# Kernel optimization log

Measured on AMD Instinct MI355X. Metric: run time of the kernel, lower is better.

Reference implementation:

```python
import jax, jax.numpy as jnp
import numpy as np

B, T, D, H, C = 32, 160, 512, 256, 6625  # batch, time, feat, gru hidden, num classes


def _gru_scan(x_proj, rk, rbias):
    """Keras GRU (reset_after=True) over time.
    x_proj: [T, B, 3H] = x @ kernel + input_bias (precomputed).
    rk: [H, 3H] recurrent kernel, rbias: [3H] recurrent bias.
    Returns hidden states [T, B, H]."""
    h0 = jnp.zeros((x_proj.shape[1], rk.shape[0]), dtype=x_proj.dtype)

    def step(h, xp):
        inner = h @ rk + rbias                 # [B, 3H]
        xz, xr, xh = jnp.split(xp, 3, axis=-1)
        rz, rr, rh = jnp.split(inner, 3, axis=-1)
        z = jax.nn.sigmoid(xz + rz)            # update gate
        r = jax.nn.sigmoid(xr + rr)            # reset gate
        hh = jnp.tanh(xh + r * rh)             # candidate
        hn = z * h + (1.0 - z) * hh
        return hn, hn

    _, hs = jax.lax.scan(step, h0, x_proj)
    return hs  # [T, B, H]


def setup_inputs() -> dict:
    key = jax.random.key(0)
    ks = jax.random.split(key, 9)
    s_in, s_rec, s_cls = 1.0 / np.sqrt(D), 1.0 / np.sqrt(H), 0.1
    return {
        "x": jax.random.normal(ks[0], (B, T, D), jnp.float32),
        "kernel_fwd": jax.random.normal(ks[1], (D, 3 * H), jnp.float32) * s_in,
        "rk_fwd": jax.random.normal(ks[2], (H, 3 * H), jnp.float32) * s_rec,
        "bias_fwd": jnp.zeros((2, 3 * H), jnp.float32),
        "kernel_bwd": jax.random.normal(ks[3], (D, 3 * H), jnp.float32) * s_in,
        "rk_bwd": jax.random.normal(ks[4], (H, 3 * H), jnp.float32) * s_rec,
        "bias_bwd": jnp.zeros((2, 3 * H), jnp.float32),
        "W": jax.random.truncated_normal(ks[5], -2.0, 2.0, (2 * H, C), jnp.float32) * s_cls,
        "b": jnp.zeros((C,), jnp.float32),
    }


def reference(x, kernel_fwd, rk_fwd, bias_fwd, kernel_bwd, rk_bwd, bias_bwd, W, b):
    x_t = jnp.transpose(x, (1, 0, 2))                       # [T, B, D]
    # forward direction
    xp_f = x_t @ kernel_fwd + bias_fwd[0]                   # [T, B, 3H]
    h_f = _gru_scan(xp_f, rk_fwd, bias_fwd[1])              # [T, B, H]
    # backward direction: run on time-reversed input, reverse output
    x_rev = x_t[::-1]
    xp_b = x_rev @ kernel_bwd + bias_bwd[0]
    h_b = _gru_scan(xp_b, rk_bwd, bias_bwd[1])[::-1]        # [T, B, H]
    out = jnp.concatenate([h_f, h_b], axis=-1)              # [T, B, 2H]
    # classifier applied per position; original reshape/matmul/reshape/transpose
    # ([B,T,2H]->[-1,2H]@W -> [B,T,C] -> [T,B,C]) is equivalent to this:
    logits = out @ W + b                                    # [T, B, C]
    return logits
```

## Files before the change

kernel.cpp:

```cpp
#include <hip/hip_runtime.h>
#include <hip/hip_bf16.h>


#define B 32
#define T 160
#define D 512
#define H 256
#define C 6625
#define H3 768
#define NT16 416
#define KP_PER_DIR 393216
#define RKB_PER_DIR 196608

typedef __attribute__((ext_vector_type(8))) short short8v;
typedef __attribute__((ext_vector_type(4))) float float4v;

__device__ inline unsigned short f2bf(float v) {
    __hip_bfloat16 b = __float2bfloat16(v);
    return *reinterpret_cast<unsigned short*>(&b);
}

__global__ __launch_bounds__(256) void pack_rkB_kernel(
    const float* __restrict__ rkf, const float* __restrict__ rkb,
    unsigned short* __restrict__ rkB)
{
    const int idx = blockIdx.x * 256 + threadIdx.x;
    const int dir = blockIdx.y;
    const float* rk = dir ? rkb : rkf;
    const int i   = idx & 7;
    const int col = (idx >> 3) & 15;
    const int kc  = (idx >> 7) & 31;
    const int nt  = idx >> 12;
    rkB[dir * RKB_PER_DIR + idx] = f2bf(rk[(kc * 8 + i) * H3 + nt * 16 + col]);
}

__global__ __launch_bounds__(256) void pack_W_kernel(
    const float* __restrict__ W, unsigned short* __restrict__ Wp)
{
    const int idx = blockIdx.x * 256 + threadIdx.x;
    const int i   = idx & 7;
    const int col = (idx >> 3) & 15;
    const int kc  = (idx >> 7) & 63;
    const int nt  = idx >> 13;
    const int k = kc * 8 + i;
    const int c = nt * 16 + col;
    const float v = (c < C) ? W[k * C + c] : 0.f;
    Wp[idx] = f2bf(v);
}

__global__ __launch_bounds__(256) void pack_xb_kernel(
    const float* __restrict__ x, unsigned short* __restrict__ xb)
{
    const int idx = blockIdx.x * 256 + threadIdx.x;
    const int k   = idx & 511;
    const int row = idx >> 9;
    const int t   = row >> 5;
    const int b   = row & 31;
    xb[idx] = f2bf(x[(b * T + t) * 512 + k]);
}

__global__ __launch_bounds__(256) void pack_kern_kernel(
    const float* __restrict__ kf, const float* __restrict__ kb,
    unsigned short* __restrict__ kernP)
{
    const int idx = blockIdx.x * 256 + threadIdx.x;
    const int dir = blockIdx.y;
    const float* kern = dir ? kb : kf;
    const int i   = idx & 7;
    const int col = (idx >> 3) & 15;
    const int kc  = (idx >> 7) & 63;
    const int nt  = idx >> 13;
    kernP[dir * KP_PER_DIR + idx] = f2bf(kern[(kc * 8 + i) * H3 + nt * 16 + col]);
}

__global__ __launch_bounds__(256) void proj_mfma_kernel(
    const unsigned short* __restrict__ xb,
    const unsigned short* __restrict__ kernP,
    const float* __restrict__ bias_f,
    const float* __restrict__ bias_b,
    float* __restrict__ xp)
{
    const int bid = blockIdx.x;
    const int ct  = bid / 40;
    const int rt  = bid % 40;
    const int dir = blockIdx.y;
    const int lane = threadIdx.x & 63;
    const int wid  = threadIdx.x >> 6;
    const int wm = wid >> 1, wn = wid & 1;
    const int rowBase = rt * 128 + wm * 64;
    const int lrow = lane & 15;
    const int lk8  = lane >> 4;
    const float* bias = dir ? bias_b : bias_f;

    float4v acc[4][4];
#pragma unroll
    for (int i = 0; i < 4; ++i)
#pragma unroll
        for (int k = 0; k < 4; ++k) acc[i][k] = (float4v){0.f, 0.f, 0.f, 0.f};

    const short* A  = (const short*)xb;
    const short* Bp = (const short*)(kernP + dir * KP_PER_DIR);
    const int ntBase = ct * 8 + wn * 4;

    int arow[4];
#pragma unroll
    for (int mt = 0; mt < 4; ++mt) {
        const int r0 = rowBase + mt * 16;
        const int s  = r0 >> 5;
        arow[mt] = (dir ? (159 - s) : s) * 32 + (r0 & 31);
    }

    for (int k0 = 0; k0 < 512; k0 += 32) {
        short8v aF[4], bF[4];
#pragma unroll
        for (int mt = 0; mt < 4; ++mt)
            aF[mt] = *(const short8v*)&A[(arow[mt] + lrow) * 512 + k0 + lk8 * 8];
#pragma unroll
        for (int ntw = 0; ntw < 4; ++ntw)
            bF[ntw] = *(const short8v*)&Bp[((ntBase + ntw) * 64 + (k0 >> 3) + lk8) * 128 + lrow * 8];
#pragma unroll
        for (int mt = 0; mt < 4; ++mt)
#pragma unroll
            for (int ntw = 0; ntw < 4; ++ntw)
                acc[mt][ntw] = __builtin_amdgcn_mfma_f32_16x16x32_bf16(
                    aF[mt], bF[ntw], acc[mt][ntw], 0, 0, 0);
    }

    const int orow = (lane >> 4) * 4;
#pragma unroll
    for (int ntw = 0; ntw < 4; ++ntw) {
        const int c = (ntBase + ntw) * 16 + lrow;
        const float bc = bias[c];
#pragma unroll
        for (int mt = 0; mt < 4; ++mt)
#pragma unroll
            for (int v = 0; v < 4; ++v)
                xp[(size_t)(dir * 5120 + rowBase + mt * 16 + orow + v) * H3 + c]
                    = acc[mt][ntw][v] + bc;
    }
}

__global__ __launch_bounds__(768, 3) void gru_scan_v6(
    const float* __restrict__ xp,
    const unsigned short* __restrict__ rkB,
    const float* __restrict__ bias_f,
    const float* __restrict__ bias_b,
    __hip_bfloat16* __restrict__ hcatb)
{
    const int bid = blockIdx.x;
    const int dir = bid >> 5;
    const int b   = bid & 31;
    const int tid = threadIdx.x;
    const int wv  = tid >> 6;
    const int lane = tid & 63;
    const int lrow = lane & 15;
    const int lk8  = lane >> 4;
    const int j   = tid & 255;
    const float* bias = dir ? bias_b : bias_f;
    const short* Bp = (const short*)(rkB + (size_t)dir * RKB_PER_DIR);

    short8v bw[32];
#pragma unroll
    for (int i = 0; i < 4; ++i)
#pragma unroll
        for (int kk = 0; kk < 8; ++kk)
            bw[i * 8 + kk] = *(const short8v*)
                &Bp[(((wv * 4 + i) * 32) + kk * 4 + lk8) * 128 + lrow * 8];

    float rbz = 0.f, rbr = 0.f, rbh = 0.f;
    if (tid < 256) {
        rbz = bias[H3 + j];
        rbr = bias[H3 + 256 + j];
        rbh = bias[H3 + 512 + j];
    }

    __shared__ float hfp[256];
    __shared__ __align__(16) unsigned short hus[256];
    __shared__ float sums[768];
    if (tid < 256) { hfp[tid] = 0.f; hus[tid] = 0; }
    __syncthreads();

    for (int s = 0; s < T; ++s) {
        float xz = 0.f, xr = 0.f, xh = 0.f;
        if (tid < 256) {
            const float* xrow = xp + ((dir * T + s) * B + b) * H3;
            xz = xrow[j];
            xr = xrow[256 + j];
            xh = xrow[512 + j];
        }

        float4v a0 = {0.f,0.f,0.f,0.f}, a1 = {0.f,0.f,0.f,0.f};
        float4v a2 = {0.f,0.f,0.f,0.f}, a3 = {0.f,0.f,0.f,0.f};
#pragma unroll
        for (int kk = 0; kk < 8; ++kk) {
            short8v aF = *(const short8v*)&hus[kk * 32 + lk8 * 8];
            a0 = __builtin_amdgcn_mfma_f32_16x16x32_bf16(aF, bw[0 * 8 + kk], a0, 0, 0, 0);
            a1 = __builtin_amdgcn_mfma_f32_16x16x32_bf16(aF, bw[1 * 8 + kk], a1, 0, 0, 0);
            a2 = __builtin_amdgcn_mfma_f32_16x16x32_bf16(aF, bw[2 * 8 + kk], a2, 0, 0, 0);
            a3 = __builtin_amdgcn_mfma_f32_16x16x32_bf16(aF, bw[3 * 8 + kk], a3, 0, 0, 0);
        }
        if (lane < 16) {
            sums[(wv * 4 + 0) * 16 + lane] = a0[0];
            sums[(wv * 4 + 1) * 16 + lane] = a1[0];
            sums[(wv * 4 + 2) * 16 + lane] = a2[0];
            sums[(wv * 4 + 3) * 16 + lane] = a3[0];
        }
        __syncthreads();

        if (tid < 256) {
            const float sz = sums[j];
            const float sr = sums[256 + j];
            const float sh = sums[512 + j];
            const float z  = 1.f / (1.f + __expf(-(xz + sz + rbz)));
            const float r  = 1.f / (1.f + __expf(-(xr + sr + rbr)));
            const float pre = xh + r * (sh + rbh);
            const float e2  = __expf(2.f * pre);
            const float hh  = 1.f - 2.f / (e2 + 1.f);
            const float hn  = z * hfp[j] + (1.f - z) * hh;
            hfp[j] = hn;
            hus[j] = f2bf(hn);
            const int ta = dir ? (T - 1 - s) : s;
            hcatb[(ta * B + b) * 512 + dir * 256 + j] = __float2bfloat16(hn);
        }
        __syncthreads();
    }
}

__global__ __launch_bounds__(256) void cls_mfma_kernel(
    const __hip_bfloat16* __restrict__ hcatb,
    const unsigned short* __restrict__ Wp,
    const float* __restrict__ bias,
    float* __restrict__ out)
{
    const int bid = blockIdx.x;
    const int ct  = bid / 40;
    const int rt  = bid % 40;
    const int lane = threadIdx.x & 63;
    const int wid  = threadIdx.x >> 6;
    const int wm = wid >> 1, wn = wid & 1;
    const int rowBase = rt * 128 + wm * 64;
    const int lrow = lane & 15;
    const int lk8  = lane >> 4;

    float4v acc[4][4];
#pragma unroll
    for (int i = 0; i < 4; ++i)
#pragma unroll
        for (int k = 0; k < 4; ++k) acc[i][k] = (float4v){0.f, 0.f, 0.f, 0.f};

    const short* A  = (const short*)hcatb;
    const short* Bp = (const short*)Wp;
    const int ntBase = ct * 8 + wn * 4;

    for (int k0 = 0; k0 < 512; k0 += 32) {
        short8v aF[4], bF[4];
#pragma unroll
        for (int mt = 0; mt < 4; ++mt)
            aF[mt] = *(const short8v*)&A[(rowBase + mt * 16 + lrow) * 512 + k0 + lk8 * 8];
#pragma unroll
        for (int ntw = 0; ntw < 4; ++ntw)
            bF[ntw] = *(const short8v*)&Bp[((ntBase + ntw) * 64 + (k0 >> 3) + lk8) * 128 + lrow * 8];
#pragma unroll
        for (int mt = 0; mt < 4; ++mt)
#pragma unroll
            for (int ntw = 0; ntw < 4; ++ntw)
                acc[mt][ntw] = __builtin_amdgcn_mfma_f32_16x16x32_bf16(
                    aF[mt], bF[ntw], acc[mt][ntw], 0, 0, 0);
    }

    const int orow = (lane >> 4) * 4;
#pragma unroll
    for (int ntw = 0; ntw < 4; ++ntw) {
        const int c = (ntBase + ntw) * 16 + lrow;
        if (c >= C) continue;
        const float bc = bias[c];
#pragma unroll
        for (int mt = 0; mt < 4; ++mt)
#pragma unroll
            for (int v = 0; v < 4; ++v)
                out[(size_t)(rowBase + mt * 16 + orow + v) * C + c] = acc[mt][ntw][v] + bc;
    }
}

__global__ __launch_bounds__(256) void proj_kernel(
    const float* __restrict__ x, const float* __restrict__ kf,
    const float* __restrict__ kb, const float* __restrict__ bias_f,
    const float* __restrict__ bias_b, float* __restrict__ xp)
{
    const int ct  = blockIdx.x;
    const int s   = blockIdx.y;
    const int dir = blockIdx.z;
    const int tid = threadIdx.x;
    const int t   = dir ? (T - 1 - s) : s;
    const float* kern = dir ? kb : kf;
    const float* bias = dir ? bias_b : bias_f;

    __shared__ float xs[32 * 512];
    for (int it = 0; it < 16; ++it) {
        int v = it * 256 + tid, row = v >> 7, k4 = v & 127;
        *(float4*)&xs[(row << 9) + (k4 << 2)] =
            *(const float4*)&x[((row * T + t) << 9) + (k4 << 2)];
    }
    __syncthreads();

    const int col = ct * 256 + tid;
    float acc[32];
#pragma unroll
    for (int r = 0; r < 32; ++r) acc[r] = 0.f;
    for (int k = 0; k < 512; k += 4) {
        float w0 = kern[(k + 0) * H3 + col];
        float w1 = kern[(k + 1) * H3 + col];
        float w2 = kern[(k + 2) * H3 + col];
        float w3 = kern[(k + 3) * H3 + col];
#pragma unroll
        for (int r = 0; r < 32; ++r) {
            float4 xv = *(const float4*)&xs[(r << 9) + k];
            acc[r] += xv.x * w0 + xv.y * w1 + xv.z * w2 + xv.w * w3;
        }
    }
    const float bb = bias[col];
    for (int r = 0; r < 32; ++r)
        xp[((dir * T + s) * B + r) * H3 + col] = acc[r] + bb;
}

__global__ __launch_bounds__(1024) void gru_scan_f32(
    const float* __restrict__ xp,
    const float* __restrict__ rk_f, const float* __restrict__ rk_b,
    const float* __restrict__ bias_f, const float* __restrict__ bias_b,
    float* __restrict__ hcat)
{
    const int bid = blockIdx.x;
    const int dir = bid >> 5;
    const int b   = bid & 31;
    const int tid = threadIdx.x;
    const int kg  = tid >> 8;
    const int j   = tid & 255;
    const int k0  = kg << 6;
    const float* rk   = dir ? rk_b : rk_f;
    const float* bias = dir ? bias_b : bias_f;
    const float rbz = bias[H3 + j];
    const float rbr = bias[H3 + 256 + j];
    const float rbh = bias[H3 + 512 + j];

    __shared__ float h[256];
    __shared__ float part[3][4][256];
    if (tid < 256) h[tid] = 0.f;
    __syncthreads();

    for (int s = 0; s < T; ++s) {
        const float* xrow = xp + ((dir * T + s) * B + b) * H3;
        float az = 0.f, ar = 0.f, ah = 0.f;
#pragma unroll 4
        for (int k = k0; k < k0 + 64; k += 4) {
            float4 h4 = *(const float4*)&h[k];
            const float* rkp = rk + k * H3 + j;
            az += h4.x * rkp[0];       ar += h4.x * rkp[256];       ah += h4.x * rkp[512];
            az += h4.y * rkp[H3];      ar += h4.y * rkp[H3+256];    ah += h4.y * rkp[H3+512];
            az += h4.z * rkp[2*H3];    ar += h4.z * rkp[2*H3+256];  ah += h4.z * rkp[2*H3+512];
            az += h4.w * rkp[3*H3];    ar += h4.w * rkp[3*H3+256];  ah += h4.w * rkp[3*H3+512];
        }
        part[0][kg][j] = az; part[1][kg][j] = ar; part[2][kg][j] = ah;
        __syncthreads();
        if (tid < 256) {
            const float sz = part[0][0][tid]+part[0][1][tid]+part[0][2][tid]+part[0][3][tid];
            const float sr = part[1][0][tid]+part[1][1][tid]+part[1][2][tid]+part[1][3][tid];
            const float sh = part[2][0][tid]+part[2][1][tid]+part[2][2][tid]+part[2][3][tid];
            const float xz = xrow[tid], xr = xrow[256+tid], xh = xrow[512+tid];
            const float z  = 1.f / (1.f + __expf(-(xz + sz + rbz)));
            const float r  = 1.f / (1.f + __expf(-(xr + sr + rbr)));
            const float pre = xh + r * (sh + rbh);
            const float e2  = __expf(2.f * pre);
            const float hh  = 1.f - 2.f / (e2 + 1.f);
            const float hn  = z * h[tid] + (1.f - z) * hh;
            h[tid] = hn;
            const int ta = dir ? (T - 1 - s) : s;
            hcat[(ta * B + b) * (2 * H) + dir * H + tid] = hn;
        }
        __syncthreads();
    }
}

__global__ __launch_bounds__(256) void cls_f32_kernel(
    const float* __restrict__ hcat, const float* __restrict__ W,
    const float* __restrict__ bias, float* __restrict__ out)
{
    const int bid = blockIdx.x;
    const int ct  = bid / 160;
    const int rt  = bid % 160;
    const int tid = threadIdx.x;
    const int r0  = rt * 32;

    __shared__ float hs[32 * 512];
    for (int it = 0; it < 16; ++it) {
        int v = it * 256 + tid, row = v >> 7, k4 = v & 127;
        *(float4*)&hs[(row << 9) + (k4 << 2)] =
            *(const float4*)&hcat[((r0 + row) << 9) + (k4 << 2)];
    }
    __syncthreads();

    const int c0 = ct * 512 + tid;
    const int c1 = c0 + 256;
    const bool v1 = (c1 < C);
    float acc0[32], acc1[32];
#pragma unroll
    for (int r = 0; r < 32; ++r) { acc0[r] = 0.f; acc1[r] = 0.f; }
    for (int k = 0; k < 512; k += 4) {
        const float* wp = W + k * C;
        float w00 = wp[c0], w01 = wp[C+c0], w02 = wp[2*C+c0], w03 = wp[3*C+c0];
        float w10 = v1 ? wp[c1] : 0.f, w11 = v1 ? wp[C+c1] : 0.f;
        float w12 = v1 ? wp[2*C+c1] : 0.f, w13 = v1 ? wp[3*C+c1] : 0.f;
#pragma unroll
        for (int r = 0; r < 32; ++r) {
            float4 hv = *(const float4*)&hs[(r << 9) + k];
            acc0[r] += hv.x*w00 + hv.y*w01 + hv.z*w02 + hv.w*w03;
            acc1[r] += hv.x*w10 + hv.y*w11 + hv.z*w12 + hv.w*w13;
        }
    }
    const float b0 = bias[c0];
    const float b1 = v1 ? bias[c1] : 0.f;
    for (int r = 0; r < 32; ++r) {
        out[(size_t)(r0+r)*C + c0] = acc0[r] + b0;
        if (v1) out[(size_t)(r0+r)*C + c1] = acc1[r] + b1;
    }
}

extern "C" void kernel_launch(void* const* d_in, const int* in_sizes, int n_in,
                              void* d_out, int out_size, void* d_ws, size_t ws_size,
                              hipStream_t stream) {
    const float* x     = (const float*)d_in[0];
    const float* kf    = (const float*)d_in[1];
    const float* rkf   = (const float*)d_in[2];
    const float* biasf = (const float*)d_in[3];
    const float* kb    = (const float*)d_in[4];
    const float* rkb   = (const float*)d_in[5];
    const float* biasb = (const float*)d_in[6];
    const float* W     = (const float*)d_in[7];
    const float* bvec  = (const float*)d_in[8];
    float* out = (float*)d_out;

    const size_t rkB_bytes   = (size_t)2 * RKB_PER_DIR * 2;
    const size_t Wp_bytes    = (size_t)NT16 * 8192 * 2;
    const size_t hcatb_bytes = (size_t)T * B * 2 * H * 2;
    const size_t planA_bytes = rkB_bytes + Wp_bytes + hcatb_bytes;

    float*          xp    = out;
    unsigned short* xb    = (unsigned short*)((char*)out + (size_t)2 * 5120 * H3 * 4);
    unsigned short* kernP = (unsigned short*)((char*)xb + (size_t)5120 * 512 * 2);

    if (ws_size >= planA_bytes) {
        char* wsb = (char*)d_ws;
        unsigned short* rkB   = (unsigned short*)wsb;
        unsigned short* Wp    = (unsigned short*)(wsb + rkB_bytes);
        __hip_bfloat16* hcatb = (__hip_bfloat16*)(wsb + rkB_bytes + Wp_bytes);

        pack_rkB_kernel<<<dim3(768, 2), 256, 0, stream>>>(rkf, rkb, rkB);
        pack_W_kernel<<<13312, 256, 0, stream>>>(W, Wp);
        pack_xb_kernel<<<10240, 256, 0, stream>>>(x, xb);
        pack_kern_kernel<<<dim3(1536, 2), 256, 0, stream>>>(kf, kb, kernP);

        proj_mfma_kernel<<<dim3(240, 2), 256, 0, stream>>>(xb, kernP, biasf, biasb, xp);

        gru_scan_v6<<<64, 768, 0, stream>>>(xp, rkB, biasf, biasb, hcatb);

        cls_mfma_kernel<<<2080, 256, 0, stream>>>(hcatb, Wp, bvec, out);
    } else {
        float* hcat = (float*)d_ws;
        dim3 g1(3, T, 2);
        proj_kernel<<<g1, 256, 0, stream>>>(x, kf, kb, biasf, biasb, xp);
        gru_scan_f32<<<64, 1024, 0, stream>>>(xp, rkf, rkb, biasf, biasb, hcat);
        cls_f32_kernel<<<13 * 160, 256, 0, stream>>>(hcat, W, bvec, out);
    }
}
```

Measured before the change: 336.9 us.

## Store input projections in bf16 and widen classifier tiles with LDS-staged activations

```diff
diff --git a/kernel.cpp b/kernel.cpp
--- a/kernel.cpp
+++ b/kernel.cpp
@@ -19,6 +19,9 @@
     __hip_bfloat16 b = __float2bfloat16(v);
     return *reinterpret_cast<unsigned short*>(&b);
 }
+__device__ inline float bf2f(unsigned short u) {
+    return __uint_as_float((unsigned int)u << 16);
+}
 
 __global__ __launch_bounds__(256) void pack_rkB_kernel(
     const float* __restrict__ rkf, const float* __restrict__ rkb,
@@ -78,7 +81,7 @@
     const unsigned short* __restrict__ kernP,
     const float* __restrict__ bias_f,
     const float* __restrict__ bias_b,
-    float* __restrict__ xp)
+    unsigned short* __restrict__ xpb)
 {
     const int bid = blockIdx.x;
     const int ct  = bid / 40;
@@ -135,13 +138,13 @@
         for (int mt = 0; mt < 4; ++mt)
 #pragma unroll
             for (int v = 0; v < 4; ++v)
-                xp[(size_t)(dir * 5120 + rowBase + mt * 16 + orow + v) * H3 + c]
-                    = acc[mt][ntw][v] + bc;
+                xpb[(size_t)(dir * 5120 + rowBase + mt * 16 + orow + v) * H3 + c]
+                    = f2bf(acc[mt][ntw][v] + bc);
     }
 }
 
 __global__ __launch_bounds__(768, 3) void gru_scan_v6(
-    const float* __restrict__ xp,
+    const unsigned short* __restrict__ xpb,
     const unsigned short* __restrict__ rkB,
     const float* __restrict__ bias_f,
     const float* __restrict__ bias_b,
@@ -183,10 +186,10 @@
     for (int s = 0; s < T; ++s) {
         float xz = 0.f, xr = 0.f, xh = 0.f;
         if (tid < 256) {
-            const float* xrow = xp + ((dir * T + s) * B + b) * H3;
-            xz = xrow[j];
-            xr = xrow[256 + j];
-            xh = xrow[512 + j];
+            const unsigned short* xrow = xpb + ((size_t)(dir * T + s) * B + b) * H3;
+            xz = bf2f(xrow[j]);
+            xr = bf2f(xrow[256 + j]);
+            xh = bf2f(xrow[512 + j]);
         }
 
         float4v a0 = {0.f,0.f,0.f,0.f}, a1 = {0.f,0.f,0.f,0.f};
@@ -226,51 +229,68 @@
     }
 }
 
-__global__ __launch_bounds__(256) void cls_mfma_kernel(
-    const __hip_bfloat16* __restrict__ hcatb,
+__global__ __launch_bounds__(256) void cls_mfma2_kernel(
+    const unsigned short* __restrict__ hcatb,
     const unsigned short* __restrict__ Wp,
     const float* __restrict__ bias,
     float* __restrict__ out)
 {
     const int bid = blockIdx.x;
-    const int ct  = bid / 40;
+    const int ctn = bid / 40;
     const int rt  = bid % 40;
-    const int lane = threadIdx.x & 63;
-    const int wid  = threadIdx.x >> 6;
+    const int tid = threadIdx.x;
+    const int lane = tid & 63;
+    const int wid  = tid >> 6;
     const int wm = wid >> 1, wn = wid & 1;
-    const int rowBase = rt * 128 + wm * 64;
     const int lrow = lane & 15;
     const int lk8  = lane >> 4;
-
-    float4v acc[4][4];
+    const int r0   = rt * 128;
+
+    __shared__ __align__(16) unsigned short As[128 * 512];
+
+    {
+        const uint4* src = (const uint4*)hcatb;
+        for (int it = 0; it < 32; ++it) {
+            const int v   = it * 256 + tid;
+            const int row = v >> 6;
+            const int c16 = (v & 63) << 4;
+            const uint4 d = src[(size_t)(r0 + row) * 64 + (v & 63)];
+            *(uint4*)((char*)As + row * 1024 + (c16 ^ ((row & 7) << 4))) = d;
+        }
+    }
+    __syncthreads();
+
+    float4v acc[4][8];
 #pragma unroll
     for (int i = 0; i < 4; ++i)
 #pragma unroll
-        for (int k = 0; k < 4; ++k) acc[i][k] = (float4v){0.f, 0.f, 0.f, 0.f};
-
-    const short* A  = (const short*)hcatb;
+        for (int k = 0; k < 8; ++k) acc[i][k] = (float4v){0.f, 0.f, 0.f, 0.f};
+
     const short* Bp = (const short*)Wp;
-    const int ntBase = ct * 8 + wn * 4;
+    const int ntBase = ctn * 16 + wn * 8;
 
     for (int k0 = 0; k0 < 512; k0 += 32) {
-        short8v aF[4], bF[4];
+        short8v aF[4], bF[8];
+#pragma unroll
+        for (int mt = 0; mt < 4; ++mt) {
+            const int row = wm * 64 + mt * 16 + lrow;
+            const int cb  = (k0 * 2 + lk8 * 16) ^ ((row & 7) << 4);
+            aF[mt] = *(const short8v*)((const char*)As + row * 1024 + cb);
+        }
+#pragma unroll
+        for (int ntw = 0; ntw < 8; ++ntw)
+            bF[ntw] = *(const short8v*)&Bp[((ntBase + ntw) * 64 + (k0 >> 3) + lk8) * 128 + lrow * 8];
 #pragma unroll
         for (int mt = 0; mt < 4; ++mt)
-            aF[mt] = *(const short8v*)&A[(rowBase + mt * 16 + lrow) * 512 + k0 + lk8 * 8];
-#pragma unroll
-        for (int ntw = 0; ntw < 4; ++ntw)
-            bF[ntw] = *(const short8v*)&Bp[((ntBase + ntw) * 64 + (k0 >> 3) + lk8) * 128 + lrow * 8];
-#pragma unroll
-        for (int mt = 0; mt < 4; ++mt)
-#pragma unroll
-            for (int ntw = 0; ntw < 4; ++ntw)
+#pragma unroll
+            for (int ntw = 0; ntw < 8; ++ntw)
                 acc[mt][ntw] = __builtin_amdgcn_mfma_f32_16x16x32_bf16(
                     aF[mt], bF[ntw], acc[mt][ntw], 0, 0, 0);
     }
 
     const int orow = (lane >> 4) * 4;
 #pragma unroll
-    for (int ntw = 0; ntw < 4; ++ntw) {
+    for (int ntw = 0; ntw < 8; ++ntw) {
         const int c = (ntBase + ntw) * 16 + lrow;
         if (c >= C) continue;
         const float bc = bias[c];
@@ -278,7 +298,8 @@
         for (int mt = 0; mt < 4; ++mt)
 #pragma unroll
             for (int v = 0; v < 4; ++v)
-                out[(size_t)(rowBase + mt * 16 + orow + v) * C + c] = acc[mt][ntw][v] + bc;
+                out[(size_t)(r0 + wm * 64 + mt * 16 + orow + v) * C + c]
+                    = acc[mt][ntw][v] + bc;
     }
 }
 
@@ -443,7 +464,7 @@
     const size_t hcatb_bytes = (size_t)T * B * 2 * H * 2;
     const size_t planA_bytes = rkB_bytes + Wp_bytes + hcatb_bytes;
 
-    float*          xp    = out;
+    unsigned short* xpb   = (unsigned short*)out;
     unsigned short* xb    = (unsigned short*)((char*)out + (size_t)2 * 5120 * H3 * 4);
     unsigned short* kernP = (unsigned short*)((char*)xb + (size_t)5120 * 512 * 2);
 
@@ -458,12 +479,14 @@
         pack_xb_kernel<<<10240, 256, 0, stream>>>(x, xb);
         pack_kern_kernel<<<dim3(1536, 2), 256, 0, stream>>>(kf, kb, kernP);
 
-        proj_mfma_kernel<<<dim3(240, 2), 256, 0, stream>>>(xb, kernP, biasf, biasb, xp);
-
-        gru_scan_v6<<<64, 768, 0, stream>>>(xp, rkB, biasf, biasb, hcatb);
-
-        cls_mfma_kernel<<<2080, 256, 0, stream>>>(hcatb, Wp, bvec, out);
+        proj_mfma_kernel<<<dim3(240, 2), 256, 0, stream>>>(xb, kernP, biasf, biasb, xpb);
+
+        gru_scan_v6<<<64, 768, 0, stream>>>(xpb, rkB, biasf, biasb, hcatb);
+
+        cls_mfma2_kernel<<<1040, 256, 0, stream>>>((const unsigned short*)hcatb,
+                                                   Wp, bvec, out);
     } else {
+        float* xp   = out;
         float* hcat = (float*)d_ws;
         dim3 g1(3, T, 2);
         proj_kernel<<<g1, 256, 0, stream>>>(x, kf, kb, biasf, biasb, xp);
```

Result: faster. 319.2 us (-5.2%).
